# Kernel optimization log

Measured on AMD Instinct MI355X. Metric: run time of the kernel, lower is better.

## Reference

```python
import jax, jax.numpy as jnp
import numpy as np
from jax import lax

VOL_RANGE = (-40.0, -40.0, -1.0, 40.0, 40.0, 5.4)
VOXEL_SIZE = 0.4
GRID_SHAPE = (200, 200, 16)  # int((hi-lo)/voxel_size) per axis
G = 1024                     # number of gaussians
C = 17                       # feature channels (semantic classes)
MAHA_THRESH = 7.5


def _make_grid_coords():
    # generate_grid(grid_shape, offset=0.5) * voxel_size + vol_range[:3]
    axes = [(jnp.arange(GRID_SHAPE[i], dtype=jnp.float32) + 0.5) * VOXEL_SIZE + VOL_RANGE[i]
            for i in range(3)]
    gx, gy, gz = jnp.meshgrid(*axes, indexing='ij')
    return jnp.stack([gx, gy, gz], axis=-1).reshape(-1, 3)  # [N, 3]


def _quat_to_rotmat(q):
    # q: [..., 4] (w, x, y, z), assumed normalized
    w, x, y, z = q[..., 0], q[..., 1], q[..., 2], q[..., 3]
    R = jnp.stack([
        1 - 2 * (y * y + z * z), 2 * (x * y - w * z), 2 * (x * z + w * y),
        2 * (x * y + w * z), 1 - 2 * (x * x + z * z), 2 * (y * z - w * x),
        2 * (x * z - w * y), 2 * (y * z + w * x), 1 - 2 * (x * x + y * y),
    ], axis=-1)
    return R.reshape(*q.shape[:-1], 3, 3)


def setup_inputs() -> dict:
    key = jax.random.key(0)
    k1, k2, k3, k4, k5 = jax.random.split(key, 5)
    lo = jnp.asarray(VOL_RANGE[:3], dtype=jnp.float32)
    hi = jnp.asarray(VOL_RANGE[3:], dtype=jnp.float32)
    means3d = lo + (hi - lo) * jax.random.uniform(k1, (1, G, 3), dtype=jnp.float32)
    opacities = jax.random.uniform(k2, (1, G, 1), dtype=jnp.float32)
    features = jax.random.normal(k3, (1, G, C), dtype=jnp.float32)
    # SPD covariances: R diag(s^2) R^T with realistic ~1m scales
    quats = jax.random.normal(k4, (1, G, 4), dtype=jnp.float32)
    quats = quats / jnp.linalg.norm(quats, axis=-1, keepdims=True)
    R = _quat_to_rotmat(quats)                                   # [1, G, 3, 3]
    scales = 0.5 + jax.random.uniform(k5, (1, G, 3), dtype=jnp.float32)  # in [0.5, 1.5] m
    covariances = jnp.einsum('bgij,bgj,bgkj->bgik', R, scales ** 2, R)
    return {
        'grid_coords': _make_grid_coords(),
        'means3d': means3d,
        'opacities': opacities,
        'features': features,
        'covariances': covariances,
    }


def _splat_one_batch(coords, means, ops, feats, covs):
    # coords: [N, 3]; means: [G, 3]; ops: [G]; feats: [G, C]; covs: [G, 3, 3]
    N = coords.shape[0]
    c = feats.shape[-1]
    inv_covs = jnp.linalg.inv(covs)  # [G, 3, 3]

    def step(carry, inp):
        dsum, fsum, cnt = carry
        mu, A, op, ft = inp
        diff = coords - mu                                  # [N, 3]
        maha = jnp.einsum('ni,ij,nj->n', diff, A, diff)     # [N]
        mask = maha <= MAHA_THRESH
        w = jnp.where(mask, op * jnp.exp(-0.5 * maha), 0.0)  # density contribution
        mf = mask.astype(coords.dtype)
        dsum = dsum + w
        fsum = fsum + mf[:, None] * (op * ft)[None, :]       # feature contribution
        cnt = cnt + mf
        return (dsum, fsum, cnt), None

    init = (jnp.zeros((N,), coords.dtype),
            jnp.zeros((N, c), coords.dtype),
            jnp.zeros((N,), coords.dtype))
    (dsum, fsum, cnt), _ = lax.scan(step, init, (means, inv_covs, ops, feats))
    # running-mean update in the torch loop == masked mean over gaussians
    denom = jnp.maximum(cnt, 1.0)
    return dsum / denom, fsum / denom[:, None]


def reference(grid_coords, means3d, opacities, features, covariances):
    dens, fts = jax.vmap(_splat_one_batch, in_axes=(None, 0, 0, 0, 0))(
        grid_coords, means3d, opacities[..., 0], features, covariances)
    B = means3d.shape[0]
    dens = dens.reshape(B, *GRID_SHAPE, 1)
    fts = fts.reshape(B, *GRID_SHAPE, features.shape[-1])
    return dens, fts
```

## Files before the change

### kernel.cpp

```cpp
#include <hip/hip_runtime.h>
#include <math.h>

#define G_N 1024
#define C_N 17
#define NX 200
#define NY 200
#define NZ 16
#define N_VOX (NX * NY * NZ)
#define MAHA_T 7.5f
#define CAP 128

__launch_bounds__(256, 4)
__global__ void gv_fused_kernel(const float* __restrict__ means,
                                const float* __restrict__ ops,
                                const float* __restrict__ feats,
                                const float* __restrict__ covs,
                                float* __restrict__ dens_out,
                                float* __restrict__ feat_out) {
    __shared__ __align__(16) char smemA[4 * 64 * C_N * 4];
    __shared__ unsigned short s_list[G_N];
    __shared__ int s_wcnt[4];

    const int tid = threadIdx.x;
    const int wave = tid >> 6;
    const int lane = tid & 63;
    const int bx = blockIdx.x, by = blockIdx.y;

    const float x0 = -40.f + (float)(bx * 4) * 0.4f;
    const float x1 = x0 + 1.6f;
    const float y0 = -40.f + (float)(by * 4) * 0.4f;
    const float y1 = y0 + 1.6f;

    unsigned short* s_stage = (unsigned short*)smemA;
    int base = 0;
#pragma unroll
    for (int r = 0; r < 4; ++r) {
        int g = wave * 256 + r * 64 + lane;
        float mx = means[3 * g], my = means[3 * g + 1], mz = means[3 * g + 2];
        float c00 = covs[9 * g], c11 = covs[9 * g + 4], c22 = covs[9 * g + 8];
        float hx = sqrtf(MAHA_T * c00) * 1.01f + 0.01f;
        float hy = sqrtf(MAHA_T * c11) * 1.01f + 0.01f;
        float hz = sqrtf(MAHA_T * c22) * 1.01f + 0.01f;
        bool hit = (mx - hx <= x1) && (mx + hx >= x0) &&
                   (my - hy <= y1) && (my + hy >= y0) &&
                   (mz - hz <= 5.4f) && (mz + hz >= -1.0f);
        unsigned long long m = __ballot(hit);
        int rank = __popcll(m & ((1ull << lane) - 1ull));
        if (hit) s_stage[wave * 256 + base + rank] = (unsigned short)g;
        base += __popcll(m);
    }
    if (lane == 0) s_wcnt[wave] = base;
    __syncthreads();
    const int c0 = s_wcnt[0], c1 = s_wcnt[1], c2 = s_wcnt[2], c3 = s_wcnt[3];
    const int total = c0 + c1 + c2 + c3;
    int off = 0;
    if (wave > 0) off += c0;
    if (wave > 1) off += c1;
    if (wave > 2) off += c2;
    for (int i = lane; i < base; i += 64)
        s_list[off + i] = s_stage[wave * 256 + i];

    const int z = lane & 15;
    const int yv = lane >> 4;
    const int X = bx * 4 + wave;
    const int Y = by * 4 + yv;
    const long n00 = (long)16 * ((long)4 * by + (long)200 * X);

    float cx, cy, cz;
    {
#pragma clang fp contract(off)
        cx = ((float)X + 0.5f) * 0.4f + -40.0f;
        cy = ((float)Y + 0.5f) * 0.4f + -40.0f;
        cz = ((float)z + 0.5f) * 0.4f + -1.0f;
    }

    float dsum = 0.f, cntf = 0.f;
    float fs[C_N];
#pragma unroll
    for (int c = 0; c < C_N; ++c) fs[c] = 0.f;

    float4* s_gd = (float4*)smemA;
    for (int cb = 0; cb < total; cb += CAP) {
        const int nc = min(CAP, total - cb);
        __syncthreads();
        if (tid < nc) {
            int g = (int)s_list[cb + tid];
            const float* cv = covs + g * 9;
            double c00 = cv[0], c01 = cv[1], c02 = cv[2];
            double c11 = cv[4], c12 = cv[5], c22 = cv[8];
            double m00 = c11 * c22 - c12 * c12;
            double m01 = c02 * c12 - c01 * c22;
            double m02 = c01 * c12 - c02 * c11;
            double det = c00 * m00 + c01 * m01 + c02 * m02;
            double inv = 1.0 / det;
            float a00 = (float)(m00 * inv);
            float a01 = (float)(m01 * inv);
            float a02 = (float)(m02 * inv);
            float a11 = (float)((c00 * c22 - c02 * c02) * inv);
            float a12 = (float)((c02 * c01 - c00 * c12) * inv);
            float a22 = (float)((c00 * c11 - c01 * c01) * inv);
            float mx = means[3 * g], my = means[3 * g + 1], mz = means[3 * g + 2];
            float op = ops[g];
            const float* ft = feats + g * C_N;
            float4* o = s_gd + tid * 8;
            o[0] = make_float4(mx, my, mz, op);
            o[1] = make_float4(a00, a11, a22, 2.f * a01);
            o[2] = make_float4(2.f * a02, 2.f * a12, op * ft[0], op * ft[1]);
            o[3] = make_float4(op * ft[2], op * ft[3], op * ft[4], op * ft[5]);
            o[4] = make_float4(op * ft[6], op * ft[7], op * ft[8], op * ft[9]);
            o[5] = make_float4(op * ft[10], op * ft[11], op * ft[12], op * ft[13]);
            o[6] = make_float4(op * ft[14], op * ft[15], op * ft[16], 0.f);
        }
        __syncthreads();
        for (int j = 0; j < nc; ++j) {
            const float4* rowp = s_gd + j * 8;
            float4 q0 = rowp[0], q1 = rowp[1], q2 = rowp[2];
            float d0 = cx - q0.x, d1 = cy - q0.y, d2 = cz - q0.z;
            float u = fmaf(q1.x, d0, fmaf(q1.w, d1, q2.x * d2));
            float v = fmaf(q1.y, d1, q2.y * d2);
            float w = q1.z * d2;
            float maha = fmaf(d0, u, fmaf(d1, v, d2 * w));
            if (maha <= MAHA_T) {
                dsum = fmaf(q0.w, __expf(-0.5f * maha), dsum);
                cntf += 1.f;
                float4 q3 = rowp[3], q4 = rowp[4], q5 = rowp[5], q6 = rowp[6];
                fs[0] += q2.z;  fs[1] += q2.w;
                fs[2] += q3.x;  fs[3] += q3.y;  fs[4] += q3.z;  fs[5] += q3.w;
                fs[6] += q4.x;  fs[7] += q4.y;  fs[8] += q4.z;  fs[9] += q4.w;
                fs[10] += q5.x; fs[11] += q5.y; fs[12] += q5.z; fs[13] += q5.w;
                fs[14] += q6.x; fs[15] += q6.y; fs[16] += q6.z;
            }
        }
    }
    __syncthreads();

    const float rd = 1.f / fmaxf(cntf, 1.f);
    dens_out[n00 + lane] = dsum * rd;

    float* fw = (float*)(smemA + wave * (64 * C_N * 4));
#pragma unroll
    for (int c = 0; c < C_N; ++c) fw[lane * C_N + c] = fs[c] * rd;
    float4* gout = (float4*)(feat_out + n00 * C_N);
    const float4* lsrc = (const float4*)fw;
#pragma unroll
    for (int r = 0; r < 4; ++r) gout[lane + 64 * r] = lsrc[lane + 64 * r];
    if (lane < 16) gout[256 + lane] = lsrc[256 + lane];
}

extern "C" void kernel_launch(void* const* d_in, const int* in_sizes, int n_in,
                              void* d_out, int out_size, void* d_ws, size_t ws_size,
                              hipStream_t stream) {
    const float* means3d     = (const float*)d_in[1];
    const float* opacities   = (const float*)d_in[2];
    const float* features    = (const float*)d_in[3];
    const float* covariances = (const float*)d_in[4];

    float* dens_out = (float*)d_out;
    float* feat_out = (float*)d_out + N_VOX;

    dim3 grid(NX / 4, NY / 4);
    gv_fused_kernel<<<grid, 256, 0, stream>>>(means3d, opacities, features,
                                              covariances, dens_out, feat_out);
}
```

Before: 24.19 us.

## Compute four voxel columns per thread to reuse each staged gaussian

Each thread now handles a 2x2 block of (x,y) columns, and each block covers an 8x8 column tile instead of 4x4, so the grid shrinks by four. Shared terms of the Mahalanobis evaluation (the z part, per-row y terms) are computed once and reused across the four voxels, and each gaussian loaded from shared memory serves more voxels. The larger tile catches more candidate gaussians per block, and the four feature accumulators raise register pressure; launch bounds drop to 2 blocks per CU to allow it. The shared row stride also goes from 8 to 7 float4s, and the epilogue writes out the four voxel groups one after another.

```diff
diff --git a/kernel.cpp b/kernel.cpp
--- a/kernel.cpp
+++ b/kernel.cpp
@@ -10,7 +10,7 @@
 #define MAHA_T 7.5f
 #define CAP 128
 
-__launch_bounds__(256, 4)
+__launch_bounds__(256, 2)
 __global__ void gv_fused_kernel(const float* __restrict__ means,
                                 const float* __restrict__ ops,
                                 const float* __restrict__ feats,
@@ -26,10 +26,10 @@
     const int lane = tid & 63;
     const int bx = blockIdx.x, by = blockIdx.y;
 
-    const float x0 = -40.f + (float)(bx * 4) * 0.4f;
-    const float x1 = x0 + 1.6f;
-    const float y0 = -40.f + (float)(by * 4) * 0.4f;
-    const float y1 = y0 + 1.6f;
+    const float x0 = -40.f + (float)(bx * 8) * 0.4f;
+    const float x1 = x0 + 3.2f;
+    const float y0 = -40.f + (float)(by * 8) * 0.4f;
+    const float y1 = y0 + 3.2f;
 
     unsigned short* s_stage = (unsigned short*)smemA;
     int base = 0;
@@ -62,22 +62,31 @@
 
     const int z = lane & 15;
     const int yv = lane >> 4;
-    const int X = bx * 4 + wave;
-    const int Y = by * 4 + yv;
-    const long n00 = (long)16 * ((long)4 * by + (long)200 * X);
+    const int X0 = bx * 8 + 2 * wave;
+    const int X1 = X0 + 1;
+    const int Ya = by * 8 + yv;
 
-    float cx, cy, cz;
+    float cx0, cx1, cya, cyb, cz;
     {
 #pragma clang fp contract(off)
-        cx = ((float)X + 0.5f) * 0.4f + -40.0f;
-        cy = ((float)Y + 0.5f) * 0.4f + -40.0f;
-        cz = ((float)z + 0.5f) * 0.4f + -1.0f;
+        cx0 = ((float)X0 + 0.5f) * 0.4f + -40.0f;
+        cx1 = ((float)X1 + 0.5f) * 0.4f + -40.0f;
+        cya = ((float)Ya + 0.5f) * 0.4f + -40.0f;
+        cyb = ((float)(Ya + 4) + 0.5f) * 0.4f + -40.0f;
+        cz  = ((float)z + 0.5f) * 0.4f + -1.0f;
     }
 
-    float dsum = 0.f, cntf = 0.f;
-    float fs[C_N];
+    float dsa = 0.f, dsb = 0.f, dsc = 0.f, dsd = 0.f;
+    float cna = 0.f, cnb = 0.f, cnc = 0.f, cnd = 0.f;
+    float fa[C_N], fb[C_N], fc[C_N], fd[C_N];
 #pragma unroll
-    for (int c = 0; c < C_N; ++c) fs[c] = 0.f;
+    for (int c = 0; c < C_N; ++c) { fa[c] = 0.f; fb[c] = 0.f; fc[c] = 0.f; fd[c] = 0.f; }
+
+#define ACC(F, DS, CN, MH) { DS = fmaf(q0.w, __expf(-0.5f * (MH)), DS); CN += 1.f; \
+    F[0] += q2.z;  F[1] += q2.w;  F[2] += q3.x;  F[3] += q3.y;  F[4] += q3.z; \
+    F[5] += q3.w;  F[6] += q4.x;  F[7] += q4.y;  F[8] += q4.z;  F[9] += q4.w; \
+    F[10] += q5.x; F[11] += q5.y; F[12] += q5.z; F[13] += q5.w; F[14] += q6.x; \
+    F[15] += q6.y; F[16] += q6.z; }
 
     float4* s_gd = (float4*)smemA;
     for (int cb = 0; cb < total; cb += CAP) {
@@ -102,7 +111,7 @@
             float mx = means[3 * g], my = means[3 * g + 1], mz = means[3 * g + 2];
             float op = ops[g];
             const float* ft = feats + g * C_N;
-            float4* o = s_gd + tid * 8;
+            float4* o = s_gd + tid * 7;
             o[0] = make_float4(mx, my, mz, op);
             o[1] = make_float4(a00, a11, a22, 2.f * a01);
             o[2] = make_float4(2.f * a02, 2.f * a12, op * ft[0], op * ft[1]);
@@ -113,38 +122,58 @@
         }
         __syncthreads();
         for (int j = 0; j < nc; ++j) {
-            const float4* rowp = s_gd + j * 8;
+            const float4* rowp = s_gd + j * 7;
             float4 q0 = rowp[0], q1 = rowp[1], q2 = rowp[2];
-            float d0 = cx - q0.x, d1 = cy - q0.y, d2 = cz - q0.z;
-            float u = fmaf(q1.x, d0, fmaf(q1.w, d1, q2.x * d2));
-            float v = fmaf(q1.y, d1, q2.y * d2);
-            float w = q1.z * d2;
-            float maha = fmaf(d0, u, fmaf(d1, v, d2 * w));
-            if (maha <= MAHA_T) {
-                dsum = fmaf(q0.w, __expf(-0.5f * maha), dsum);
-                cntf += 1.f;
+            float d0a = cx0 - q0.x, d0b = cx1 - q0.x;
+            float d1a = cya - q0.y, d1b = cyb - q0.y;
+            float d2  = cz - q0.z;
+            float s1 = q2.x * d2;
+            float s2 = q2.y * d2;
+            float w  = q1.z * d2;
+            float sw = d2 * w;
+            float va = fmaf(q1.y, d1a, s2);
+            float vb = fmaf(q1.y, d1b, s2);
+            float ta = fmaf(d1a, va, sw);
+            float tb = fmaf(d1b, vb, sw);
+            float uaa = fmaf(q1.x, d0a, fmaf(q1.w, d1a, s1));
+            float uab = fmaf(q1.x, d0a, fmaf(q1.w, d1b, s1));
+            float uba = fmaf(q1.x, d0b, fmaf(q1.w, d1a, s1));
+            float ubb = fmaf(q1.x, d0b, fmaf(q1.w, d1b, s1));
+            float mA = fmaf(d0a, uaa, ta);
+            float mB = fmaf(d0a, uab, tb);
+            float mC = fmaf(d0b, uba, ta);
+            float mD = fmaf(d0b, ubb, tb);
+            bool ha = mA <= MAHA_T, hb = mB <= MAHA_T;
+            bool hc = mC <= MAHA_T, hd = mD <= MAHA_T;
+            if (ha | hb | hc | hd) {
                 float4 q3 = rowp[3], q4 = rowp[4], q5 = rowp[5], q6 = rowp[6];
-                fs[0] += q2.z;  fs[1] += q2.w;
-                fs[2] += q3.x;  fs[3] += q3.y;  fs[4] += q3.z;  fs[5] += q3.w;
-                fs[6] += q4.x;  fs[7] += q4.y;  fs[8] += q4.z;  fs[9] += q4.w;
-                fs[10] += q5.x; fs[11] += q5.y; fs[12] += q5.z; fs[13] += q5.w;
-                fs[14] += q6.x; fs[15] += q6.y; fs[16] += q6.z;
+                if (ha) ACC(fa, dsa, cna, mA);
+                if (hb) ACC(fb, dsb, cnb, mB);
+                if (hc) ACC(fc, dsc, cnc, mC);
+                if (hd) ACC(fd, dsd, cnd, mD);
             }
         }
     }
     __syncthreads();
 
-    const float rd = 1.f / fmaxf(cntf, 1.f);
-    dens_out[n00 + lane] = dsum * rd;
+    float* fw = (float*)(smemA + wave * (64 * C_N * 4));
+    const float4* lsrc = (const float4*)fw;
 
-    float* fw = (float*)(smemA + wave * (64 * C_N * 4));
-#pragma unroll
-    for (int c = 0; c < C_N; ++c) fw[lane * C_N + c] = fs[c] * rd;
-    float4* gout = (float4*)(feat_out + n00 * C_N);
-    const float4* lsrc = (const float4*)fw;
-#pragma unroll
-    for (int r = 0; r < 4; ++r) gout[lane + 64 * r] = lsrc[lane + 64 * r];
-    if (lane < 16) gout[256 + lane] = lsrc[256 + lane];
+#define EPI(F, DS, CN, XX, HH) { \
+    const float rd = 1.f / fmaxf(CN, 1.f); \
+    const long nb = (long)16 * ((long)(by * 8 + 4 * (HH)) + 200L * (XX)); \
+    dens_out[nb + lane] = DS * rd; \
+    _Pragma("unroll") \
+    for (int c = 0; c < C_N; ++c) fw[lane * C_N + c] = F[c] * rd; \
+    float4* gout = (float4*)(feat_out + nb * C_N); \
+    _Pragma("unroll") \
+    for (int r = 0; r < 4; ++r) gout[lane + 64 * r] = lsrc[lane + 64 * r]; \
+    if (lane < 16) gout[256 + lane] = lsrc[256 + lane]; }
+
+    EPI(fa, dsa, cna, X0, 0);
+    EPI(fb, dsb, cnb, X0, 1);
+    EPI(fc, dsc, cnc, X1, 0);
+    EPI(fd, dsd, cnd, X1, 1);
 }
 
 extern "C" void kernel_launch(void* const* d_in, const int* in_sizes, int n_in,
@@ -158,7 +187,7 @@
     float* dens_out = (float*)d_out;
     float* feat_out = (float*)d_out + N_VOX;
 
-    dim3 grid(NX / 4, NY / 4);
+    dim3 grid(NX / 8, NY / 8);
     gv_fused_kernel<<<grid, 256, 0, stream>>>(means3d, opacities, features,
                                               covariances, dens_out, feat_out);
 }
```

Measured after the change: 20.45 us. -15.5%, faster.

## Enlarge block tile to 8x8 columns and reuse staged gaussian data across subtiles

Applied to the files above, without the earlier changes.

Each block now covers an 8x8 column footprint instead of 4x4, processed as four 2x8 sub-tiles. When the candidate list fits in one chunk, the inverted covariance, mean and feature data staged in shared memory is computed once and reused across all sub-tiles. The staging row stride shrinks from 8 to 7 float4s, and the output buffer gets its own shared region. In exchange the coarser culling box admits more gaussians per voxel, and the grid drops to 625 blocks, which lowers parallelism on the device.

```diff
diff --git a/kernel.cpp b/kernel.cpp
--- a/kernel.cpp
+++ b/kernel.cpp
@@ -17,8 +17,9 @@
                                 const float* __restrict__ covs,
                                 float* __restrict__ dens_out,
                                 float* __restrict__ feat_out) {
-    __shared__ __align__(16) char smemA[4 * 64 * C_N * 4];
     __shared__ unsigned short s_list[G_N];
+    __shared__ __align__(16) float4 s_gd[CAP * 7];
+    __shared__ __align__(16) float  s_out[4 * 64 * C_N];
     __shared__ int s_wcnt[4];
 
     const int tid = threadIdx.x;
@@ -26,12 +27,12 @@
     const int lane = tid & 63;
     const int bx = blockIdx.x, by = blockIdx.y;
 
-    const float x0 = -40.f + (float)(bx * 4) * 0.4f;
-    const float x1 = x0 + 1.6f;
-    const float y0 = -40.f + (float)(by * 4) * 0.4f;
-    const float y1 = y0 + 1.6f;
+    const float x0 = -40.f + (float)(bx * 8) * 0.4f;
+    const float x1 = x0 + 3.2f;
+    const float y0 = -40.f + (float)(by * 8) * 0.4f;
+    const float y1 = y0 + 3.2f;
 
-    unsigned short* s_stage = (unsigned short*)smemA;
+    unsigned short* s_stage = (unsigned short*)s_gd;
     int base = 0;
 #pragma unroll
     for (int r = 0; r < 4; ++r) {
@@ -60,91 +61,102 @@
     for (int i = lane; i < base; i += 64)
         s_list[off + i] = s_stage[wave * 256 + i];
 
-    const int z = lane & 15;
-    const int yv = lane >> 4;
-    const int X = bx * 4 + wave;
-    const int Y = by * 4 + yv;
-    const long n00 = (long)16 * ((long)4 * by + (long)200 * X);
+    const int nchunks = (total + CAP - 1) / CAP;
 
-    float cx, cy, cz;
+    const int z = tid & 15;
+    const int yv = (tid >> 4) & 7;
+    const int xh = tid >> 7;
+    const int Y = by * 8 + yv;
+
+    float cy, cz;
     {
 #pragma clang fp contract(off)
-        cx = ((float)X + 0.5f) * 0.4f + -40.0f;
         cy = ((float)Y + 0.5f) * 0.4f + -40.0f;
         cz = ((float)z + 0.5f) * 0.4f + -1.0f;
     }
 
-    float dsum = 0.f, cntf = 0.f;
-    float fs[C_N];
+#define ACC(F, DS, CN, MH) { DS = fmaf(q0.w, __expf(-0.5f * (MH)), DS); CN += 1.f; \
+    F[0] += q2.z;  F[1] += q2.w;  F[2] += q3.x;  F[3] += q3.y;  F[4] += q3.z; \
+    F[5] += q3.w;  F[6] += q4.x;  F[7] += q4.y;  F[8] += q4.z;  F[9] += q4.w; \
+    F[10] += q5.x; F[11] += q5.y; F[12] += q5.z; F[13] += q5.w; F[14] += q6.x; \
+    F[15] += q6.y; F[16] += q6.z; }
+
+    for (int s = 0; s < 4; ++s) {
+        const int X = bx * 8 + 2 * s + xh;
+        float cx;
+        {
+#pragma clang fp contract(off)
+            cx = ((float)X + 0.5f) * 0.4f + -40.0f;
+        }
+
+        float ds = 0.f, cn = 0.f;
+        float fs[C_N];
 #pragma unroll
-    for (int c = 0; c < C_N; ++c) fs[c] = 0.f;
+        for (int c = 0; c < C_N; ++c) fs[c] = 0.f;
 
-    float4* s_gd = (float4*)smemA;
-    for (int cb = 0; cb < total; cb += CAP) {
-        const int nc = min(CAP, total - cb);
-        __syncthreads();
-        if (tid < nc) {
-            int g = (int)s_list[cb + tid];
-            const float* cv = covs + g * 9;
-            double c00 = cv[0], c01 = cv[1], c02 = cv[2];
-            double c11 = cv[4], c12 = cv[5], c22 = cv[8];
-            double m00 = c11 * c22 - c12 * c12;
-            double m01 = c02 * c12 - c01 * c22;
-            double m02 = c01 * c12 - c02 * c11;
-            double det = c00 * m00 + c01 * m01 + c02 * m02;
-            double inv = 1.0 / det;
-            float a00 = (float)(m00 * inv);
-            float a01 = (float)(m01 * inv);
-            float a02 = (float)(m02 * inv);
-            float a11 = (float)((c00 * c22 - c02 * c02) * inv);
-            float a12 = (float)((c02 * c01 - c00 * c12) * inv);
-            float a22 = (float)((c00 * c11 - c01 * c01) * inv);
-            float mx = means[3 * g], my = means[3 * g + 1], mz = means[3 * g + 2];
-            float op = ops[g];
-            const float* ft = feats + g * C_N;
-            float4* o = s_gd + tid * 8;
-            o[0] = make_float4(mx, my, mz, op);
-            o[1] = make_float4(a00, a11, a22, 2.f * a01);
-            o[2] = make_float4(2.f * a02, 2.f * a12, op * ft[0], op * ft[1]);
-            o[3] = make_float4(op * ft[2], op * ft[3], op * ft[4], op * ft[5]);
-            o[4] = make_float4(op * ft[6], op * ft[7], op * ft[8], op * ft[9]);
-            o[5] = make_float4(op * ft[10], op * ft[11], op * ft[12], op * ft[13]);
-            o[6] = make_float4(op * ft[14], op * ft[15], op * ft[16], 0.f);
-        }
-        __syncthreads();
-        for (int j = 0; j < nc; ++j) {
-            const float4* rowp = s_gd + j * 8;
-            float4 q0 = rowp[0], q1 = rowp[1], q2 = rowp[2];
-            float d0 = cx - q0.x, d1 = cy - q0.y, d2 = cz - q0.z;
-            float u = fmaf(q1.x, d0, fmaf(q1.w, d1, q2.x * d2));
-            float v = fmaf(q1.y, d1, q2.y * d2);
-            float w = q1.z * d2;
-            float maha = fmaf(d0, u, fmaf(d1, v, d2 * w));
-            if (maha <= MAHA_T) {
-                dsum = fmaf(q0.w, __expf(-0.5f * maha), dsum);
-                cntf += 1.f;
-                float4 q3 = rowp[3], q4 = rowp[4], q5 = rowp[5], q6 = rowp[6];
-                fs[0] += q2.z;  fs[1] += q2.w;
-                fs[2] += q3.x;  fs[3] += q3.y;  fs[4] += q3.z;  fs[5] += q3.w;
-                fs[6] += q4.x;  fs[7] += q4.y;  fs[8] += q4.z;  fs[9] += q4.w;
-                fs[10] += q5.x; fs[11] += q5.y; fs[12] += q5.z; fs[13] += q5.w;
-                fs[14] += q6.x; fs[15] += q6.y; fs[16] += q6.z;
+        for (int cb = 0; cb < total; cb += CAP) {
+            const int nc = min(CAP, total - cb);
+            if (nchunks > 1 || s == 0) {
+                __syncthreads();
+                if (tid < nc) {
+                    int g = (int)s_list[cb + tid];
+                    const float* cv = covs + g * 9;
+                    double c00 = cv[0], c01 = cv[1], c02 = cv[2];
+                    double c11 = cv[4], c12 = cv[5], c22 = cv[8];
+                    double m00 = c11 * c22 - c12 * c12;
+                    double m01 = c02 * c12 - c01 * c22;
+                    double m02 = c01 * c12 - c02 * c11;
+                    double det = c00 * m00 + c01 * m01 + c02 * m02;
+                    double inv = 1.0 / det;
+                    float a00 = (float)(m00 * inv);
+                    float a01 = (float)(m01 * inv);
+                    float a02 = (float)(m02 * inv);
+                    float a11 = (float)((c00 * c22 - c02 * c02) * inv);
+                    float a12 = (float)((c02 * c01 - c00 * c12) * inv);
+                    float a22 = (float)((c00 * c11 - c01 * c01) * inv);
+                    float mx = means[3 * g], my = means[3 * g + 1], mz = means[3 * g + 2];
+                    float op = ops[g];
+                    const float* ft = feats + g * C_N;
+                    float4* o = s_gd + tid * 7;
+                    o[0] = make_float4(mx, my, mz, op);
+                    o[1] = make_float4(a00, a11, a22, 2.f * a01);
+                    o[2] = make_float4(2.f * a02, 2.f * a12, op * ft[0], op * ft[1]);
+                    o[3] = make_float4(op * ft[2], op * ft[3], op * ft[4], op * ft[5]);
+                    o[4] = make_float4(op * ft[6], op * ft[7], op * ft[8], op * ft[9]);
+                    o[5] = make_float4(op * ft[10], op * ft[11], op * ft[12], op * ft[13]);
+                    o[6] = make_float4(op * ft[14], op * ft[15], op * ft[16], 0.f);
+                }
+                __syncthreads();
+            }
+            for (int j = 0; j < nc; ++j) {
+                const float4* rowp = s_gd + j * 7;
+                float4 q0 = rowp[0], q1 = rowp[1], q2 = rowp[2];
+                float d0 = cx - q0.x, d1 = cy - q0.y, d2 = cz - q0.z;
+                float u = fmaf(q1.x, d0, fmaf(q1.w, d1, q2.x * d2));
+                float v = fmaf(q1.y, d1, q2.y * d2);
+                float w = q1.z * d2;
+                float maha = fmaf(d0, u, fmaf(d1, v, d2 * w));
+                if (maha <= MAHA_T) {
+                    float4 q3 = rowp[3], q4 = rowp[4], q5 = rowp[5], q6 = rowp[6];
+                    ACC(fs, ds, cn, maha);
+                }
             }
         }
+
+        const float rd = 1.f / fmaxf(cn, 1.f);
+        const int Xw = bx * 8 + 2 * s + (wave >> 1);
+        const int n0 = 16 * ((by * 8 + 4 * (wave & 1)) + 200 * Xw);
+        dens_out[n0 + lane] = ds * rd;
+
+        float* fw = s_out + wave * (64 * C_N);
+        const float4* lsrc = (const float4*)fw;
+#pragma unroll
+        for (int c = 0; c < C_N; ++c) fw[lane * C_N + c] = fs[c] * rd;
+        float4* gout = (float4*)(feat_out + (long)n0 * C_N);
+#pragma unroll
+        for (int r = 0; r < 4; ++r) gout[lane + 64 * r] = lsrc[lane + 64 * r];
+        if (lane < 16) gout[256 + lane] = lsrc[256 + lane];
     }
-    __syncthreads();
-
-    const float rd = 1.f / fmaxf(cntf, 1.f);
-    dens_out[n00 + lane] = dsum * rd;
-
-    float* fw = (float*)(smemA + wave * (64 * C_N * 4));
-#pragma unroll
-    for (int c = 0; c < C_N; ++c) fw[lane * C_N + c] = fs[c] * rd;
-    float4* gout = (float4*)(feat_out + n00 * C_N);
-    const float4* lsrc = (const float4*)fw;
-#pragma unroll
-    for (int r = 0; r < 4; ++r) gout[lane + 64 * r] = lsrc[lane + 64 * r];
-    if (lane < 16) gout[256 + lane] = lsrc[256 + lane];
 }
 
 extern "C" void kernel_launch(void* const* d_in, const int* in_sizes, int n_in,
@@ -158,7 +170,7 @@
     float* dens_out = (float*)d_out;
     float* feat_out = (float*)d_out + N_VOX;
 
-    dim3 grid(NX / 4, NY / 4);
+    dim3 grid(NX / 8, NY / 8);
     gv_fused_kernel<<<grid, 256, 0, stream>>>(means3d, opacities, features,
                                               covariances, dens_out, feat_out);
 }
```

New measurement: 27.50 us. 1.14x slower.
